# Optimization experiments

Hardware: AMD Instinct MI355X
Metric: run time of the kernel (lower is better)

Reference implementation:

```python
import jax, jax.numpy as jnp
import numpy as np

STATE_DIM, ACTION_DIM, HIDDEN, ACTOR_HIDDEN = 64, 8, 256, 256
B, T = 1024, 512


def _uniform(key, shape, bound):
    return jax.random.uniform(key, shape, jnp.float32, -bound, bound)


def setup_inputs() -> dict:
    key = jax.random.key(0)
    ks = jax.random.split(key, 12)
    k = 1.0 / np.sqrt(HIDDEN)  # PyTorch GRU/Linear init bound
    ka = 1.0 / np.sqrt(ACTOR_HIDDEN)
    return {
        "x_seq": jax.random.normal(ks[0], (B, T, STATE_DIM), jnp.float32),
        # GRU params (PyTorch layout: [3*H, in] with gate order r,z,n)
        "w_ih": _uniform(ks[1], (3 * HIDDEN, STATE_DIM), k),
        "w_hh": _uniform(ks[2], (3 * HIDDEN, HIDDEN), k),
        "b_ih": _uniform(ks[3], (3 * HIDDEN,), k),
        "b_hh": _uniform(ks[4], (3 * HIDDEN,), k),
        # base MLP
        "w_base": _uniform(ks[5], (ACTOR_HIDDEN, HIDDEN), k),
        "b_base": _uniform(ks[6], (ACTOR_HIDDEN,), k),
        # factorized heads
        "w_dir": _uniform(ks[7], (ACTION_DIM, ACTOR_HIDDEN), ka),
        "b_dir": _uniform(ks[8], (ACTION_DIM,), ka),
        "w_mag": _uniform(ks[9], (ACTION_DIM, ACTOR_HIDDEN), ka),
        "b_mag": _uniform(ks[10], (ACTION_DIM,), ka),
    }


def reference(x_seq, w_ih, w_hh, b_ih, b_hh, w_base, b_base, w_dir, b_dir, w_mag, b_mag):
    H = w_hh.shape[1]

    def step(h, x_t):
        gi = x_t @ w_ih.T + b_ih          # [B, 3H]
        gh = h @ w_hh.T + b_hh            # [B, 3H]
        i_r, i_z, i_n = jnp.split(gi, 3, axis=-1)
        h_r, h_z, h_n = jnp.split(gh, 3, axis=-1)
        r = jax.nn.sigmoid(i_r + h_r)
        z = jax.nn.sigmoid(i_z + h_z)
        n = jnp.tanh(i_n + r * h_n)
        h_new = (1.0 - z) * n + z * h
        return h_new, None

    h0 = jnp.zeros((x_seq.shape[0], H), x_seq.dtype)
    last, _ = jax.lax.scan(step, h0, jnp.swapaxes(x_seq, 0, 1))  # carry = h_T
    h = jax.nn.relu(last @ w_base.T + b_base)
    direction = jnp.tanh(h @ w_dir.T + b_dir)
    magnitude = jax.nn.sigmoid(h @ w_mag.T + b_mag)
    return direction * magnitude
```

## Files before the change

kernel.cpp:

```cpp
#include <hip/hip_runtime.h>

#define T_SEQ 512
#define HID 256

typedef _Float16 half8 __attribute__((ext_vector_type(8)));
typedef _Float16 half4 __attribute__((ext_vector_type(4)));
typedef float floatx4 __attribute__((ext_vector_type(4)));

#define OFF_GH 0
#define OFF_GI (OFF_GH + 384 * 512)
#define OFF_WB (OFF_GI + 96 * 512)
#define OFF_WD (OFF_WB + 128 * 512)
#define HSAVE_OFF_BYTES (4ull << 20)
#define GI_OFF_BYTES (6ull << 20)

#define MFMA16(A, B, C) __builtin_amdgcn_mfma_f32_16x16x32_f16(A, B, C, 0, 0, 0)

__device__ __forceinline__ float sigm(float x) { return 1.0f / (1.0f + __expf(-x)); }
__device__ __forceinline__ float tanh_fast(float x) {
  float e = __expf(2.0f * x);
  return 1.0f - 2.0f / (e + 1.0f);
}

__global__ void prep_kernel(const float* __restrict__ w_ih,
                            const float* __restrict__ w_hh,
                            const float* __restrict__ w_base,
                            const float* __restrict__ w_dir,
                            const float* __restrict__ w_mag,
                            _Float16* __restrict__ ws) {
  const int f = blockIdx.x;
  const int lane = threadIdx.x;
  const int col = lane & 15, quad = lane >> 4;
  const float* src;
  int n, k, ld;
  _Float16* dst;
  if (f < 384) {
    int nt = f % 6, kt = (f / 6) % 8, w = f / 48;
    n = (nt >> 1) * 256 + w * 32 + (nt & 1) * 16 + col;
    k = kt * 32 + quad * 8;
    src = w_hh; ld = 256;
    dst = ws + OFF_GH + ((w * 8 + kt) * 6 + nt) * 512 + lane * 8;
  } else if (f < 480) {
    int f2 = f - 384;
    int nt = f2 % 6, kt = (f2 / 6) % 2, w = f2 / 12;
    n = (nt >> 1) * 256 + w * 32 + (nt & 1) * 16 + col;
    k = kt * 32 + quad * 8;
    src = w_ih; ld = 64;
    dst = ws + OFF_GI + ((w * 2 + kt) * 6 + nt) * 512 + lane * 8;
  } else if (f < 608) {
    int f3 = f - 480;
    int nt = f3 % 2, kt = (f3 / 2) % 8, w = f3 / 16;
    n = w * 32 + nt * 16 + col;
    k = kt * 32 + quad * 8;
    src = w_base; ld = 256;
    dst = ws + OFF_WB + ((w * 8 + kt) * 2 + nt) * 512 + lane * 8;
  } else {
    int kt = f - 608;
    k = kt * 32 + quad * 8;
    ld = 256;
    if (col < 8) { src = w_dir; n = col; } else { src = w_mag; n = col - 8; }
    dst = ws + OFF_WD + kt * 512 + lane * 8;
  }
#pragma unroll
  for (int j = 0; j < 8; ++j)
    dst[j] = (_Float16)src[n * ld + k + j];
}

__global__ __launch_bounds__(512, 1)
void gi_prepass_kernel(const float* __restrict__ x_seq,
                       const float* __restrict__ b_ih,
                       const float* __restrict__ b_hh,
                       const _Float16* __restrict__ ws,
                       uint2* __restrict__ gi_out,
                       int t0, int nTq, int chunk) {
  const int tid = threadIdx.x;
  const int lane = tid & 63;
  const int w = tid >> 6;
  const int col = lane & 15;
  const int quad = lane >> 4;
  const int btile = blockIdx.x / nTq, tq = blockIdx.x % nTq;
  const int row0 = btile * 16;
  const int tstart = t0 + tq * 32;

  const half8* __restrict__ gip = (const half8*)(ws + OFF_GI) + w * (12 * 64);
  half8 wg[12];
#pragma unroll
  for (int f = 0; f < 12; ++f) wg[f] = gip[f * 64 + lane];

  float bias[6];
#pragma unroll
  for (int a = 0; a < 6; ++a) {
    const int c = w * 32 + (a & 1) * 16 + col;
    const int g = a >> 1;
    bias[a] = (g < 2) ? (b_ih[g * 256 + c] + b_hh[g * 256 + c]) : b_ih[512 + c];
  }

  const float* const xlane = x_seq + (size_t)(row0 + col) * (T_SEQ * 64) + quad * 8;
  uint2* const gout = gi_out + (size_t)btile * ((size_t)chunk * 3072) +
                      (size_t)w * 384 + lane;

  float4 xc[4], xn[4];
  {
    const float* p = xlane + (size_t)tstart * 64;
    xc[0] = *(const float4*)(p);
    xc[1] = *(const float4*)(p + 4);
    xc[2] = *(const float4*)(p + 32);
    xc[3] = *(const float4*)(p + 36);
  }

#pragma unroll 1
  for (int tt = 0; tt < 32; ++tt) {
    const int t = tstart + tt;
    if (tt + 1 < 32) {
      const float* p = xlane + (size_t)(t + 1) * 64;
      xn[0] = *(const float4*)(p);
      xn[1] = *(const float4*)(p + 4);
      xn[2] = *(const float4*)(p + 32);
      xn[3] = *(const float4*)(p + 36);
    }
    half8 ax0, ax1;
#pragma unroll
    for (int j = 0; j < 4; ++j) {
      ax0[j]     = (_Float16)((const float*)&xc[0])[j];
      ax0[4 + j] = (_Float16)((const float*)&xc[1])[j];
      ax1[j]     = (_Float16)((const float*)&xc[2])[j];
      ax1[4 + j] = (_Float16)((const float*)&xc[3])[j];
    }

    floatx4 acc[6];
#pragma unroll
    for (int a = 0; a < 6; ++a) acc[a] = (floatx4){0.f, 0.f, 0.f, 0.f};
#pragma unroll
    for (int nt = 0; nt < 6; ++nt) {
      acc[nt] = MFMA16(ax0, wg[nt], acc[nt]);
      acc[nt] = MFMA16(ax1, wg[6 + nt], acc[nt]);
    }

    uint2* gp = gout + (size_t)(t - t0) * 3072;
#pragma unroll
    for (int a = 0; a < 6; ++a) {
      union { uint2 u; half4 h; } pk;
#pragma unroll
      for (int r2 = 0; r2 < 4; ++r2)
        pk.h[r2] = (_Float16)(acc[a][r2] + bias[a]);
      gp[a * 64] = pk.u;
    }
#pragma unroll
    for (int i = 0; i < 4; ++i) xc[i] = xn[i];
  }
}

__global__ __launch_bounds__(512, 1)
void gru_main_kernel(const float* __restrict__ b_hh,
                     const float* __restrict__ b_base,
                     const float* __restrict__ b_dir,
                     const float* __restrict__ b_mag,
                     const _Float16* __restrict__ ws,
                     const uint2* __restrict__ gi_in,
                     float* __restrict__ hsave,
                     float* __restrict__ out,
                     int chunk, int first, int last) {
  __shared__ __align__(16) _Float16 hlin[2][4096];

  const int tid = threadIdx.x;
  const int lane = tid & 63;
  const int w = tid >> 6;
  const int col = lane & 15;
  const int quad = lane >> 4;
  const int row0 = blockIdx.x * 16;

  float bhn[2];
#pragma unroll
  for (int s = 0; s < 2; ++s) bhn[s] = b_hh[512 + w * 32 + s * 16 + col];

  float hreg[2][4];
  if (first) {
#pragma unroll
    for (int s = 0; s < 2; ++s)
#pragma unroll
      for (int r2 = 0; r2 < 4; ++r2) hreg[s][r2] = 0.0f;
    *(half8*)&hlin[0][tid * 8] = (half8)((_Float16)0.0f);
  } else {
    const float* hp = hsave + ((size_t)blockIdx.x * 512 + tid) * 8;
#pragma unroll
    for (int s = 0; s < 2; ++s) {
      const int inner = s * 16 + col;
      const int widx = w * 512 + (inner >> 3) * 128 + (col & 7);
#pragma unroll
      for (int r2 = 0; r2 < 4; ++r2) {
        hreg[s][r2] = hp[s * 4 + r2];
        hlin[0][widx + (quad * 4 + r2) * 8] = (_Float16)hreg[s][r2];
      }
    }
  }

  const half8* __restrict__ ghp = (const half8*)(ws + OFF_GH) + w * (48 * 64);
  const half8* __restrict__ wbp = (const half8*)(ws + OFF_WB) + w * (16 * 64);
  const half8* __restrict__ wdp = (const half8*)(ws + OFF_WD);

  half8 wreg[40];
#pragma unroll
  for (int f = 0; f < 40; ++f) wreg[f] = ghp[f * 64 + lane];

  const uint2* const gilane =
      gi_in + (size_t)blockIdx.x * ((size_t)chunk * 3072) + (size_t)w * 384 + lane;

#pragma unroll 1
  for (int tl = 0; tl < chunk; ++tl) {
    __syncthreads();
    const int cur = tl & 1;
    const _Float16* hc = hlin[cur];
    _Float16* hn = hlin[cur ^ 1];

    uint2 g[6];
    const uint2* gp = gilane + (size_t)tl * 3072;
#pragma unroll
    for (int a = 0; a < 6; ++a) g[a] = gp[a * 64];

    half8 st[8];
#pragma unroll
    for (int i = 0; i < 8; ++i) st[i] = ghp[(40 + i) * 64 + lane];

    half8 ah[8];
#pragma unroll
    for (int kt = 0; kt < 8; ++kt)
      ah[kt] = *(const half8*)&hc[kt * 512 + lane * 8];

    floatx4 acc[6];
#pragma unroll
    for (int a = 0; a < 6; ++a) acc[a] = (floatx4){0.f, 0.f, 0.f, 0.f};

#pragma unroll
    for (int f = 0; f < 40; ++f)
      acc[f % 6] = MFMA16(ah[f / 6], wreg[f], acc[f % 6]);
#pragma unroll
    for (int i = 0; i < 8; ++i) {
      const int f = 40 + i;
      acc[f % 6] = MFMA16(ah[f / 6], st[i], acc[f % 6]);
    }

#pragma unroll
    for (int s = 0; s < 2; ++s) {
      const int inner = s * 16 + col;
      const int widx = w * 512 + (inner >> 3) * 128 + (col & 7);
      union { uint2 u; half4 h; } gr, gz, gn;
      gr.u = g[0 + s]; gz.u = g[2 + s]; gn.u = g[4 + s];
#pragma unroll
      for (int r2 = 0; r2 < 4; ++r2) {
        const float rr = sigm(acc[0 + s][r2] + (float)gr.h[r2]);
        const float zz = sigm(acc[2 + s][r2] + (float)gz.h[r2]);
        const float nn = tanh_fast((float)gn.h[r2] + rr * (acc[4 + s][r2] + bhn[s]));
        const float hnew = zz * hreg[s][r2] + (1.0f - zz) * nn;
        hreg[s][r2] = hnew;
        hn[widx + (quad * 4 + r2) * 8] = (_Float16)hnew;
      }
    }
  }

  if (!last) {
    float* hp = hsave + ((size_t)blockIdx.x * 512 + tid) * 8;
#pragma unroll
    for (int s = 0; s < 2; ++s)
#pragma unroll
      for (int r2 = 0; r2 < 4; ++r2) hp[s * 4 + r2] = hreg[s][r2];
    return;
  }

  __syncthreads();
  {
    floatx4 ab[2];
    ab[0] = (floatx4){0.f, 0.f, 0.f, 0.f};
    ab[1] = (floatx4){0.f, 0.f, 0.f, 0.f};
#pragma unroll
    for (int kt = 0; kt < 8; ++kt) {
      const half8 ahh = *(const half8*)&hlin[0][kt * 512 + lane * 8];
      const half8* bp = wbp + kt * (2 * 64) + lane;
      ab[0] = MFMA16(ahh, bp[0],  ab[0]);
      ab[1] = MFMA16(ahh, bp[64], ab[1]);
    }
#pragma unroll
    for (int s = 0; s < 2; ++s) {
      const int inner = s * 16 + col;
      const int widx = w * 512 + (inner >> 3) * 128 + (col & 7);
      const float bb = b_base[w * 32 + inner];
#pragma unroll
      for (int r2 = 0; r2 < 4; ++r2) {
        const float v = ab[s][r2] + bb;
        hlin[1][widx + (quad * 4 + r2) * 8] = (_Float16)fmaxf(v, 0.0f);
      }
    }
  }
  __syncthreads();

  if (w == 0) {
    floatx4 ad = (floatx4){0.f, 0.f, 0.f, 0.f};
#pragma unroll
    for (int kt = 0; kt < 8; ++kt) {
      const half8 ahh = *(const half8*)&hlin[1][kt * 512 + lane * 8];
      ad = MFMA16(ahh, wdp[kt * 64 + lane], ad);
    }
    const float bd = (col < 8) ? b_dir[col] : b_mag[col - 8];
#pragma unroll
    for (int r2 = 0; r2 < 4; ++r2) {
      const float v = ad[r2] + bd;
      const float act = (col < 8) ? tanh_fast(v) : sigm(v);
      const float other = __shfl_xor(act, 8, 64);
      if (col < 8)
        out[(size_t)(row0 + quad * 4 + r2) * 8 + col] = act * other;
    }
  }
}

__global__ __launch_bounds__(512, 2)
void gru_head_fallback(const float* __restrict__ x_seq,
                       const float* __restrict__ b_ih,
                       const float* __restrict__ b_hh,
                       const float* __restrict__ b_base,
                       const float* __restrict__ b_dir,
                       const float* __restrict__ b_mag,
                       const _Float16* __restrict__ ws,
                       float* __restrict__ out) {
  __shared__ __align__(16) _Float16 hlin[2][4096];
  __shared__ __align__(16) _Float16 wlds[8][4096];

  const int tid = threadIdx.x;
  const int lane = tid & 63;
  const int w = tid >> 6;
  const int col = lane & 15;
  const int quad = lane >> 4;
  const int row0 = blockIdx.x * 16;

  *(half8*)&hlin[0][tid * 8] = (half8)((_Float16)0.0f);

  float br[2], bz[2], bin_[2], bhn[2];
#pragma unroll
  for (int s = 0; s < 2; ++s) {
    const int c = w * 32 + s * 16 + col;
    br[s] = b_ih[c] + b_hh[c];
    bz[s] = b_ih[256 + c] + b_hh[256 + c];
    bin_[s] = b_ih[512 + c];
    bhn[s] = b_hh[512 + c];
  }
  float hreg[2][4];
#pragma unroll
  for (int s = 0; s < 2; ++s)
#pragma unroll
    for (int r2 = 0; r2 < 4; ++r2) hreg[s][r2] = 0.0f;

  const half8* __restrict__ ghp = (const half8*)(ws + OFF_GH) + w * (48 * 64);
  const half8* __restrict__ gip = (const half8*)(ws + OFF_GI) + w * (12 * 64);
  const half8* __restrict__ wbp = (const half8*)(ws + OFF_WB) + w * (16 * 64);
  const half8* __restrict__ wdp = (const half8*)(ws + OFF_WD);

  half8 wreg[16];
#pragma unroll
  for (int f = 0; f < 16; ++f) wreg[f] = ghp[f * 64 + lane];
  _Float16* const wlw = wlds[w];
#pragma unroll
  for (int j = 0; j < 8; ++j)
    *(half8*)&wlw[j * 512 + lane * 8] = ghp[(16 + j) * 64 + lane];

  const float* const xlane = x_seq + ((size_t)(row0 + col) * T_SEQ) * 64 + quad * 8;
  float4 xc[4], xn[4];
  {
    const float* p = xlane;
    xc[0] = *(const float4*)(p);
    xc[1] = *(const float4*)(p + 4);
    xc[2] = *(const float4*)(p + 32);
    xc[3] = *(const float4*)(p + 36);
  }

  auto body = [&](int t, int tpre, int cur, float4* xcur, float4* xnext) {
    const int nxt = cur ^ 1;
    __syncthreads();
    half8 s1[6], s2[6];
#pragma unroll
    for (int i = 0; i < 6; ++i) s1[i] = ghp[(24 + i) * 64 + lane];
#pragma unroll
    for (int i = 0; i < 6; ++i) s2[i] = ghp[(30 + i) * 64 + lane];
    {
      const float* p = xlane + (size_t)tpre * 64;
      xnext[0] = *(const float4*)(p);
      xnext[1] = *(const float4*)(p + 4);
      xnext[2] = *(const float4*)(p + 32);
      xnext[3] = *(const float4*)(p + 36);
    }
    half8 ah[8];
#pragma unroll
    for (int kt = 0; kt < 8; ++kt)
      ah[kt] = *(const half8*)&hlin[cur][kt * 512 + lane * 8];
    half8 wl[8];
#pragma unroll
    for (int j = 0; j < 8; ++j)
      wl[j] = *(const half8*)&wlw[j * 512 + lane * 8];
    half8 ax0, ax1;
#pragma unroll
    for (int j = 0; j < 4; ++j) {
      ax0[j]     = (_Float16)((const float*)&xcur[0])[j];
      ax0[4 + j] = (_Float16)((const float*)&xcur[1])[j];
      ax1[j]     = (_Float16)((const float*)&xcur[2])[j];
      ax1[4 + j] = (_Float16)((const float*)&xcur[3])[j];
    }
    floatx4 acc[8];
#pragma unroll
    for (int i = 0; i < 8; ++i) acc[i] = (floatx4){0.f, 0.f, 0.f, 0.f};
#pragma unroll
    for (int f = 0; f < 16; ++f)
      acc[f % 6] = MFMA16(ah[f / 6], wreg[f], acc[f % 6]);
    half8 s3[6];
#pragma unroll
    for (int i = 0; i < 6; ++i) s3[i] = ghp[(36 + i) * 64 + lane];
#pragma unroll
    for (int j = 0; j < 8; ++j) {
      const int f = 16 + j;
      acc[f % 6] = MFMA16(ah[f / 6], wl[j], acc[f % 6]);
    }
#pragma unroll
    for (int i = 0; i < 6; ++i) {
      const int f = 24 + i;
      acc[f % 6] = MFMA16(ah[f / 6], s1[i], acc[f % 6]);
    }
    half8 s4[6];
#pragma unroll
    for (int i = 0; i < 6; ++i) s4[i] = ghp[(42 + i) * 64 + lane];
#pragma unroll
    for (int i = 0; i < 6; ++i) {
      const int f = 30 + i;
      acc[f % 6] = MFMA16(ah[f / 6], s2[i], acc[f % 6]);
    }
    half8 s5[6];
#pragma unroll
    for (int i = 0; i < 6; ++i) s5[i] = gip[i * 64 + lane];
#pragma unroll
    for (int i = 0; i < 6; ++i) {
      const int f = 36 + i;
      acc[f % 6] = MFMA16(ah[f / 6], s3[i], acc[f % 6]);
    }
    half8 s6[6];
#pragma unroll
    for (int i = 0; i < 6; ++i) s6[i] = gip[(6 + i) * 64 + lane];
#pragma unroll
    for (int i = 0; i < 6; ++i) {
      const int f = 42 + i;
      acc[f % 6] = MFMA16(ah[f / 6], s4[i], acc[f % 6]);
    }
#pragma unroll
    for (int i = 0; i < 6; ++i) {
      const int aidx = (i < 4) ? i : i + 2;
      acc[aidx] = MFMA16(ax0, s5[i], acc[aidx]);
    }
#pragma unroll
    for (int i = 0; i < 6; ++i) {
      const int aidx = (i < 4) ? i : i + 2;
      acc[aidx] = MFMA16(ax1, s6[i], acc[aidx]);
    }
#pragma unroll
    for (int s = 0; s < 2; ++s) {
      const int inner = s * 16 + col;
      const int widx = w * 512 + (inner >> 3) * 128 + (col & 7);
#pragma unroll
      for (int r2 = 0; r2 < 4; ++r2) {
        const float rr = sigm(acc[0 + s][r2] + br[s]);
        const float zz = sigm(acc[2 + s][r2] + bz[s]);
        const float nn = tanh_fast(acc[6 + s][r2] + bin_[s] + rr * (acc[4 + s][r2] + bhn[s]));
        const float hnew = zz * hreg[s][r2] + (1.0f - zz) * nn;
        hreg[s][r2] = hnew;
        hlin[nxt][widx + (quad * 4 + r2) * 8] = (_Float16)hnew;
      }
    }
  };

#pragma unroll 1
  for (int t = 0; t < T_SEQ; t += 2) {
    body(t, t + 1, 0, xc, xn);
    const int tp2 = (t + 2 < T_SEQ) ? (t + 2) : (T_SEQ - 1);
    body(t + 1, tp2, 1, xn, xc);
  }

  __syncthreads();
  {
    floatx4 ab[2];
    ab[0] = (floatx4){0.f, 0.f, 0.f, 0.f};
    ab[1] = (floatx4){0.f, 0.f, 0.f, 0.f};
#pragma unroll
    for (int kt = 0; kt < 8; ++kt) {
      const half8 ahh = *(const half8*)&hlin[0][kt * 512 + lane * 8];
      const half8* bp = wbp + kt * (2 * 64) + lane;
      ab[0] = MFMA16(ahh, bp[0],  ab[0]);
      ab[1] = MFMA16(ahh, bp[64], ab[1]);
    }
#pragma unroll
    for (int s = 0; s < 2; ++s) {
      const int inner = s * 16 + col;
      const int widx = w * 512 + (inner >> 3) * 128 + (col & 7);
      const float bb = b_base[w * 32 + inner];
#pragma unroll
      for (int r2 = 0; r2 < 4; ++r2) {
        const float v = ab[s][r2] + bb;
        hlin[1][widx + (quad * 4 + r2) * 8] = (_Float16)fmaxf(v, 0.0f);
      }
    }
  }
  __syncthreads();
  if (w == 0) {
    floatx4 ad = (floatx4){0.f, 0.f, 0.f, 0.f};
#pragma unroll
    for (int kt = 0; kt < 8; ++kt) {
      const half8 ahh = *(const half8*)&hlin[1][kt * 512 + lane * 8];
      ad = MFMA16(ahh, wdp[kt * 64 + lane], ad);
    }
    const float bd = (col < 8) ? b_dir[col] : b_mag[col - 8];
#pragma unroll
    for (int r2 = 0; r2 < 4; ++r2) {
      const float v = ad[r2] + bd;
      const float act = (col < 8) ? tanh_fast(v) : sigm(v);
      const float other = __shfl_xor(act, 8, 64);
      if (col < 8)
        out[(size_t)(row0 + quad * 4 + r2) * 8 + col] = act * other;
    }
  }
}

extern "C" void kernel_launch(void* const* d_in, const int* in_sizes, int n_in,
                              void* d_out, int out_size, void* d_ws, size_t ws_size,
                              hipStream_t stream) {
  const float* x_seq  = (const float*)d_in[0];
  const float* b_ih   = (const float*)d_in[3];
  const float* b_hh   = (const float*)d_in[4];
  const float* b_base = (const float*)d_in[6];
  const float* b_dir  = (const float*)d_in[8];
  const float* b_mag  = (const float*)d_in[10];
  _Float16* ws = (_Float16*)d_ws;
  float* out = (float*)d_out;

  hipLaunchKernelGGL(prep_kernel, dim3(616), dim3(64), 0, stream,
                     (const float*)d_in[1], (const float*)d_in[2],
                     (const float*)d_in[5], (const float*)d_in[7],
                     (const float*)d_in[9], ws);

  int chunk = 0;
  const int cand[3] = {128, 64, 32};
  for (int i = 0; i < 3; ++i) {
    const size_t need = GI_OFF_BYTES + 64ull * (size_t)cand[i] * 3072ull * 8ull;
    if (ws_size >= need) { chunk = cand[i]; break; }
  }

  if (chunk) {
    uint2* gi = (uint2*)((char*)d_ws + GI_OFF_BYTES);
    float* hsave = (float*)((char*)d_ws + HSAVE_OFF_BYTES);
    const int nchunks = T_SEQ / chunk;
    const int nTq = chunk / 32;
    for (int c = 0; c < nchunks; ++c) {
      hipLaunchKernelGGL(gi_prepass_kernel, dim3(64 * nTq), dim3(512), 0, stream,
                         x_seq, b_ih, b_hh, ws, gi, c * chunk, nTq, chunk);
      hipLaunchKernelGGL(gru_main_kernel, dim3(64), dim3(512), 0, stream,
                         b_hh, b_base, b_dir, b_mag, ws, gi, hsave, out,
                         chunk, (c == 0) ? 1 : 0, (c == nchunks - 1) ? 1 : 0);
    }
  } else {
    hipLaunchKernelGGL(gru_head_fallback, dim3(64), dim3(512), 0, stream,
                       x_seq, b_ih, b_hh, b_base, b_dir, b_mag, ws, out);
  }
}
```

Measured before the change: 1.912 ms.

## Fuse input projection into single persistent GRU kernel, drop chunked prepass

Replaces the chunked scheme, which alternated an input-projection prepass kernel with a recurrent kernel and staged gate inputs and hidden state through global memory, with one kernel of 64 blocks. That kernel computes x_t·W_ih with MFMA inside each timestep, keeps 40 of the 48 W_hh fragments plus all W_ih fragments in registers, streams the remaining 8 from global memory, and raises wave priority around the MFMA block. This removes the many kernel launches and the global round trips for gi and the saved hidden state. In exchange, every serial step now carries extra MFMAs and x loads on the critical path, and register pressure rises.

```diff
diff --git a/kernel.cpp b/kernel.cpp
--- a/kernel.cpp
+++ b/kernel.cpp
@@ -11,8 +11,6 @@
 #define OFF_GI (OFF_GH + 384 * 512)
 #define OFF_WB (OFF_GI + 96 * 512)
 #define OFF_WD (OFF_WB + 128 * 512)
-#define HSAVE_OFF_BYTES (4ull << 20)
-#define GI_OFF_BYTES (6ull << 20)
 
 #define MFMA16(A, B, C) __builtin_amdgcn_mfma_f32_16x16x32_f16(A, B, C, 0, 0, 0)
 
@@ -67,99 +65,14 @@
 }
 
 __global__ __launch_bounds__(512, 1)
-void gi_prepass_kernel(const float* __restrict__ x_seq,
-                       const float* __restrict__ b_ih,
-                       const float* __restrict__ b_hh,
-                       const _Float16* __restrict__ ws,
-                       uint2* __restrict__ gi_out,
-                       int t0, int nTq, int chunk) {
-  const int tid = threadIdx.x;
-  const int lane = tid & 63;
-  const int w = tid >> 6;
-  const int col = lane & 15;
-  const int quad = lane >> 4;
-  const int btile = blockIdx.x / nTq, tq = blockIdx.x % nTq;
-  const int row0 = btile * 16;
-  const int tstart = t0 + tq * 32;
-
-  const half8* __restrict__ gip = (const half8*)(ws + OFF_GI) + w * (12 * 64);
-  half8 wg[12];
-#pragma unroll
-  for (int f = 0; f < 12; ++f) wg[f] = gip[f * 64 + lane];
-
-  float bias[6];
-#pragma unroll
-  for (int a = 0; a < 6; ++a) {
-    const int c = w * 32 + (a & 1) * 16 + col;
-    const int g = a >> 1;
-    bias[a] = (g < 2) ? (b_ih[g * 256 + c] + b_hh[g * 256 + c]) : b_ih[512 + c];
-  }
-
-  const float* const xlane = x_seq + (size_t)(row0 + col) * (T_SEQ * 64) + quad * 8;
-  uint2* const gout = gi_out + (size_t)btile * ((size_t)chunk * 3072) +
-                      (size_t)w * 384 + lane;
-
-  float4 xc[4], xn[4];
-  {
-    const float* p = xlane + (size_t)tstart * 64;
-    xc[0] = *(const float4*)(p);
-    xc[1] = *(const float4*)(p + 4);
-    xc[2] = *(const float4*)(p + 32);
-    xc[3] = *(const float4*)(p + 36);
-  }
-
-#pragma unroll 1
-  for (int tt = 0; tt < 32; ++tt) {
-    const int t = tstart + tt;
-    if (tt + 1 < 32) {
-      const float* p = xlane + (size_t)(t + 1) * 64;
-      xn[0] = *(const float4*)(p);
-      xn[1] = *(const float4*)(p + 4);
-      xn[2] = *(const float4*)(p + 32);
-      xn[3] = *(const float4*)(p + 36);
-    }
-    half8 ax0, ax1;
-#pragma unroll
-    for (int j = 0; j < 4; ++j) {
-      ax0[j]     = (_Float16)((const float*)&xc[0])[j];
-      ax0[4 + j] = (_Float16)((const float*)&xc[1])[j];
-      ax1[j]     = (_Float16)((const float*)&xc[2])[j];
-      ax1[4 + j] = (_Float16)((const float*)&xc[3])[j];
-    }
-
-    floatx4 acc[6];
-#pragma unroll
-    for (int a = 0; a < 6; ++a) acc[a] = (floatx4){0.f, 0.f, 0.f, 0.f};
-#pragma unroll
-    for (int nt = 0; nt < 6; ++nt) {
-      acc[nt] = MFMA16(ax0, wg[nt], acc[nt]);
-      acc[nt] = MFMA16(ax1, wg[6 + nt], acc[nt]);
-    }
-
-    uint2* gp = gout + (size_t)(t - t0) * 3072;
-#pragma unroll
-    for (int a = 0; a < 6; ++a) {
-      union { uint2 u; half4 h; } pk;
-#pragma unroll
-      for (int r2 = 0; r2 < 4; ++r2)
-        pk.h[r2] = (_Float16)(acc[a][r2] + bias[a]);
-      gp[a * 64] = pk.u;
-    }
-#pragma unroll
-    for (int i = 0; i < 4; ++i) xc[i] = xn[i];
-  }
-}
-
-__global__ __launch_bounds__(512, 1)
-void gru_main_kernel(const float* __restrict__ b_hh,
-                     const float* __restrict__ b_base,
-                     const float* __restrict__ b_dir,
-                     const float* __restrict__ b_mag,
-                     const _Float16* __restrict__ ws,
-                     const uint2* __restrict__ gi_in,
-                     float* __restrict__ hsave,
-                     float* __restrict__ out,
-                     int chunk, int first, int last) {
+void gru_all_kernel(const float* __restrict__ x_seq,
+                    const float* __restrict__ b_ih,
+                    const float* __restrict__ b_hh,
+                    const float* __restrict__ b_base,
+                    const float* __restrict__ b_dir,
+                    const float* __restrict__ b_mag,
+                    const _Float16* __restrict__ ws,
+                    float* __restrict__ out) {
   __shared__ __align__(16) _Float16 hlin[2][4096];
 
   const int tid = threadIdx.x;
@@ -169,169 +82,6 @@
   const int quad = lane >> 4;
   const int row0 = blockIdx.x * 16;
 
-  float bhn[2];
-#pragma unroll
-  for (int s = 0; s < 2; ++s) bhn[s] = b_hh[512 + w * 32 + s * 16 + col];
-
-  float hreg[2][4];
-  if (first) {
-#pragma unroll
-    for (int s = 0; s < 2; ++s)
-#pragma unroll
-      for (int r2 = 0; r2 < 4; ++r2) hreg[s][r2] = 0.0f;
-    *(half8*)&hlin[0][tid * 8] = (half8)((_Float16)0.0f);
-  } else {
-    const float* hp = hsave + ((size_t)blockIdx.x * 512 + tid) * 8;
-#pragma unroll
-    for (int s = 0; s < 2; ++s) {
-      const int inner = s * 16 + col;
-      const int widx = w * 512 + (inner >> 3) * 128 + (col & 7);
-#pragma unroll
-      for (int r2 = 0; r2 < 4; ++r2) {
-        hreg[s][r2] = hp[s * 4 + r2];
-        hlin[0][widx + (quad * 4 + r2) * 8] = (_Float16)hreg[s][r2];
-      }
-    }
-  }
-
-  const half8* __restrict__ ghp = (const half8*)(ws + OFF_GH) + w * (48 * 64);
-  const half8* __restrict__ wbp = (const half8*)(ws + OFF_WB) + w * (16 * 64);
-  const half8* __restrict__ wdp = (const half8*)(ws + OFF_WD);
-
-  half8 wreg[40];
-#pragma unroll
-  for (int f = 0; f < 40; ++f) wreg[f] = ghp[f * 64 + lane];
-
-  const uint2* const gilane =
-      gi_in + (size_t)blockIdx.x * ((size_t)chunk * 3072) + (size_t)w * 384 + lane;
-
-#pragma unroll 1
-  for (int tl = 0; tl < chunk; ++tl) {
-    __syncthreads();
-    const int cur = tl & 1;
-    const _Float16* hc = hlin[cur];
-    _Float16* hn = hlin[cur ^ 1];
-
-    uint2 g[6];
-    const uint2* gp = gilane + (size_t)tl * 3072;
-#pragma unroll
-    for (int a = 0; a < 6; ++a) g[a] = gp[a * 64];
-
-    half8 st[8];
-#pragma unroll
-    for (int i = 0; i < 8; ++i) st[i] = ghp[(40 + i) * 64 + lane];
-
-    half8 ah[8];
-#pragma unroll
-    for (int kt = 0; kt < 8; ++kt)
-      ah[kt] = *(const half8*)&hc[kt * 512 + lane * 8];
-
-    floatx4 acc[6];
-#pragma unroll
-    for (int a = 0; a < 6; ++a) acc[a] = (floatx4){0.f, 0.f, 0.f, 0.f};
-
-#pragma unroll
-    for (int f = 0; f < 40; ++f)
-      acc[f % 6] = MFMA16(ah[f / 6], wreg[f], acc[f % 6]);
-#pragma unroll
-    for (int i = 0; i < 8; ++i) {
-      const int f = 40 + i;
-      acc[f % 6] = MFMA16(ah[f / 6], st[i], acc[f % 6]);
-    }
-
-#pragma unroll
-    for (int s = 0; s < 2; ++s) {
-      const int inner = s * 16 + col;
-      const int widx = w * 512 + (inner >> 3) * 128 + (col & 7);
-      union { uint2 u; half4 h; } gr, gz, gn;
-      gr.u = g[0 + s]; gz.u = g[2 + s]; gn.u = g[4 + s];
-#pragma unroll
-      for (int r2 = 0; r2 < 4; ++r2) {
-        const float rr = sigm(acc[0 + s][r2] + (float)gr.h[r2]);
-        const float zz = sigm(acc[2 + s][r2] + (float)gz.h[r2]);
-        const float nn = tanh_fast((float)gn.h[r2] + rr * (acc[4 + s][r2] + bhn[s]));
-        const float hnew = zz * hreg[s][r2] + (1.0f - zz) * nn;
-        hreg[s][r2] = hnew;
-        hn[widx + (quad * 4 + r2) * 8] = (_Float16)hnew;
-      }
-    }
-  }
-
-  if (!last) {
-    float* hp = hsave + ((size_t)blockIdx.x * 512 + tid) * 8;
-#pragma unroll
-    for (int s = 0; s < 2; ++s)
-#pragma unroll
-      for (int r2 = 0; r2 < 4; ++r2) hp[s * 4 + r2] = hreg[s][r2];
-    return;
-  }
-
-  __syncthreads();
-  {
-    floatx4 ab[2];
-    ab[0] = (floatx4){0.f, 0.f, 0.f, 0.f};
-    ab[1] = (floatx4){0.f, 0.f, 0.f, 0.f};
-#pragma unroll
-    for (int kt = 0; kt < 8; ++kt) {
-      const half8 ahh = *(const half8*)&hlin[0][kt * 512 + lane * 8];
-      const half8* bp = wbp + kt * (2 * 64) + lane;
-      ab[0] = MFMA16(ahh, bp[0],  ab[0]);
-      ab[1] = MFMA16(ahh, bp[64], ab[1]);
-    }
-#pragma unroll
-    for (int s = 0; s < 2; ++s) {
-      const int inner = s * 16 + col;
-      const int widx = w * 512 + (inner >> 3) * 128 + (col & 7);
-      const float bb = b_base[w * 32 + inner];
-#pragma unroll
-      for (int r2 = 0; r2 < 4; ++r2) {
-        const float v = ab[s][r2] + bb;
-        hlin[1][widx + (quad * 4 + r2) * 8] = (_Float16)fmaxf(v, 0.0f);
-      }
-    }
-  }
-  __syncthreads();
-
-  if (w == 0) {
-    floatx4 ad = (floatx4){0.f, 0.f, 0.f, 0.f};
-#pragma unroll
-    for (int kt = 0; kt < 8; ++kt) {
-      const half8 ahh = *(const half8*)&hlin[1][kt * 512 + lane * 8];
-      ad = MFMA16(ahh, wdp[kt * 64 + lane], ad);
-    }
-    const float bd = (col < 8) ? b_dir[col] : b_mag[col - 8];
-#pragma unroll
-    for (int r2 = 0; r2 < 4; ++r2) {
-      const float v = ad[r2] + bd;
-      const float act = (col < 8) ? tanh_fast(v) : sigm(v);
-      const float other = __shfl_xor(act, 8, 64);
-      if (col < 8)
-        out[(size_t)(row0 + quad * 4 + r2) * 8 + col] = act * other;
-    }
-  }
-}
-
-__global__ __launch_bounds__(512, 2)
-void gru_head_fallback(const float* __restrict__ x_seq,
-                       const float* __restrict__ b_ih,
-                       const float* __restrict__ b_hh,
-                       const float* __restrict__ b_base,
-                       const float* __restrict__ b_dir,
-                       const float* __restrict__ b_mag,
-                       const _Float16* __restrict__ ws,
-                       float* __restrict__ out) {
-  __shared__ __align__(16) _Float16 hlin[2][4096];
-  __shared__ __align__(16) _Float16 wlds[8][4096];
-
-  const int tid = threadIdx.x;
-  const int lane = tid & 63;
-  const int w = tid >> 6;
-  const int col = lane & 15;
-  const int quad = lane >> 4;
-  const int row0 = blockIdx.x * 16;
-
-  *(half8*)&hlin[0][tid * 8] = (half8)((_Float16)0.0f);
-
   float br[2], bz[2], bin_[2], bhn[2];
 #pragma unroll
   for (int s = 0; s < 2; ++s) {
@@ -341,26 +91,28 @@
     bin_[s] = b_ih[512 + c];
     bhn[s] = b_hh[512 + c];
   }
+
   float hreg[2][4];
 #pragma unroll
   for (int s = 0; s < 2; ++s)
 #pragma unroll
     for (int r2 = 0; r2 < 4; ++r2) hreg[s][r2] = 0.0f;
+  *(half8*)&hlin[0][tid * 8] = (half8)((_Float16)0.0f);
 
   const half8* __restrict__ ghp = (const half8*)(ws + OFF_GH) + w * (48 * 64);
   const half8* __restrict__ gip = (const half8*)(ws + OFF_GI) + w * (12 * 64);
   const half8* __restrict__ wbp = (const half8*)(ws + OFF_WB) + w * (16 * 64);
   const half8* __restrict__ wdp = (const half8*)(ws + OFF_WD);
 
-  half8 wreg[16];
-#pragma unroll
-  for (int f = 0; f < 16; ++f) wreg[f] = ghp[f * 64 + lane];
-  _Float16* const wlw = wlds[w];
-#pragma unroll
-  for (int j = 0; j < 8; ++j)
-    *(half8*)&wlw[j * 512 + lane * 8] = ghp[(16 + j) * 64 + lane];
-
-  const float* const xlane = x_seq + ((size_t)(row0 + col) * T_SEQ) * 64 + quad * 8;
+  half8 wreg[40];
+#pragma unroll
+  for (int f = 0; f < 40; ++f) wreg[f] = ghp[f * 64 + lane];
+  half8 wg[12];
+#pragma unroll
+  for (int f = 0; f < 12; ++f) wg[f] = gip[f * 64 + lane];
+
+  const float* const xlane =
+      x_seq + (size_t)(row0 + col) * (T_SEQ * 64) + quad * 8;
   float4 xc[4], xn[4];
   {
     const float* p = xlane;
@@ -370,14 +122,14 @@
     xc[3] = *(const float4*)(p + 36);
   }
 
-  auto body = [&](int t, int tpre, int cur, float4* xcur, float4* xnext) {
-    const int nxt = cur ^ 1;
+  auto body = [&](int tpre, int cur, float4* xcur, float4* xnext) {
     __syncthreads();
-    half8 s1[6], s2[6];
-#pragma unroll
-    for (int i = 0; i < 6; ++i) s1[i] = ghp[(24 + i) * 64 + lane];
-#pragma unroll
-    for (int i = 0; i < 6; ++i) s2[i] = ghp[(30 + i) * 64 + lane];
+    const _Float16* hc = hlin[cur];
+    _Float16* hn = hlin[cur ^ 1];
+
+    half8 st[8];
+#pragma unroll
+    for (int i = 0; i < 8; ++i) st[i] = ghp[(40 + i) * 64 + lane];
     {
       const float* p = xlane + (size_t)tpre * 64;
       xnext[0] = *(const float4*)(p);
@@ -385,14 +137,12 @@
       xnext[2] = *(const float4*)(p + 32);
       xnext[3] = *(const float4*)(p + 36);
     }
+
     half8 ah[8];
 #pragma unroll
     for (int kt = 0; kt < 8; ++kt)
-      ah[kt] = *(const half8*)&hlin[cur][kt * 512 + lane * 8];
-    half8 wl[8];
-#pragma unroll
-    for (int j = 0; j < 8; ++j)
-      wl[j] = *(const half8*)&wlw[j * 512 + lane * 8];
+      ah[kt] = *(const half8*)&hc[kt * 512 + lane * 8];
+
     half8 ax0, ax1;
 #pragma unroll
     for (int j = 0; j < 4; ++j) {
@@ -401,59 +151,31 @@
       ax1[j]     = (_Float16)((const float*)&xcur[2])[j];
       ax1[4 + j] = (_Float16)((const float*)&xcur[3])[j];
     }
+
     floatx4 acc[8];
 #pragma unroll
     for (int i = 0; i < 8; ++i) acc[i] = (floatx4){0.f, 0.f, 0.f, 0.f};
-#pragma unroll
-    for (int f = 0; f < 16; ++f)
+
+    __builtin_amdgcn_s_setprio(1);
+#pragma unroll
+    for (int f = 0; f < 40; ++f)
       acc[f % 6] = MFMA16(ah[f / 6], wreg[f], acc[f % 6]);
-    half8 s3[6];
-#pragma unroll
-    for (int i = 0; i < 6; ++i) s3[i] = ghp[(36 + i) * 64 + lane];
-#pragma unroll
-    for (int j = 0; j < 8; ++j) {
-      const int f = 16 + j;
-      acc[f % 6] = MFMA16(ah[f / 6], wl[j], acc[f % 6]);
-    }
-#pragma unroll
-    for (int i = 0; i < 6; ++i) {
-      const int f = 24 + i;
-      acc[f % 6] = MFMA16(ah[f / 6], s1[i], acc[f % 6]);
-    }
-    half8 s4[6];
-#pragma unroll
-    for (int i = 0; i < 6; ++i) s4[i] = ghp[(42 + i) * 64 + lane];
-#pragma unroll
-    for (int i = 0; i < 6; ++i) {
-      const int f = 30 + i;
-      acc[f % 6] = MFMA16(ah[f / 6], s2[i], acc[f % 6]);
-    }
-    half8 s5[6];
-#pragma unroll
-    for (int i = 0; i < 6; ++i) s5[i] = gip[i * 64 + lane];
-#pragma unroll
-    for (int i = 0; i < 6; ++i) {
-      const int f = 36 + i;
-      acc[f % 6] = MFMA16(ah[f / 6], s3[i], acc[f % 6]);
-    }
-    half8 s6[6];
-#pragma unroll
-    for (int i = 0; i < 6; ++i) s6[i] = gip[(6 + i) * 64 + lane];
-#pragma unroll
-    for (int i = 0; i < 6; ++i) {
-      const int f = 42 + i;
-      acc[f % 6] = MFMA16(ah[f / 6], s4[i], acc[f % 6]);
-    }
-#pragma unroll
-    for (int i = 0; i < 6; ++i) {
-      const int aidx = (i < 4) ? i : i + 2;
-      acc[aidx] = MFMA16(ax0, s5[i], acc[aidx]);
-    }
-#pragma unroll
-    for (int i = 0; i < 6; ++i) {
-      const int aidx = (i < 4) ? i : i + 2;
-      acc[aidx] = MFMA16(ax1, s6[i], acc[aidx]);
-    }
+#pragma unroll
+    for (int kt2 = 0; kt2 < 2; ++kt2) {
+      const half8 ax = kt2 ? ax1 : ax0;
+#pragma unroll
+      for (int nt = 0; nt < 6; ++nt) {
+        const int aidx = (nt < 4) ? nt : nt + 2;
+        acc[aidx] = MFMA16(ax, wg[kt2 * 6 + nt], acc[aidx]);
+      }
+    }
+#pragma unroll
+    for (int i = 0; i < 8; ++i) {
+      const int f = 40 + i;
+      acc[f % 6] = MFMA16(ah[f / 6], st[i], acc[f % 6]);
+    }
+    __builtin_amdgcn_s_setprio(0);
+
 #pragma unroll
     for (int s = 0; s < 2; ++s) {
       const int inner = s * 16 + col;
@@ -462,19 +184,20 @@
       for (int r2 = 0; r2 < 4; ++r2) {
         const float rr = sigm(acc[0 + s][r2] + br[s]);
         const float zz = sigm(acc[2 + s][r2] + bz[s]);
-        const float nn = tanh_fast(acc[6 + s][r2] + bin_[s] + rr * (acc[4 + s][r2] + bhn[s]));
+        const float nn =
+            tanh_fast(acc[6 + s][r2] + bin_[s] + rr * (acc[4 + s][r2] + bhn[s]));
         const float hnew = zz * hreg[s][r2] + (1.0f - zz) * nn;
         hreg[s][r2] = hnew;
-        hlin[nxt][widx + (quad * 4 + r2) * 8] = (_Float16)hnew;
+        hn[widx + (quad * 4 + r2) * 8] = (_Float16)hnew;
       }
     }
   };
 
 #pragma unroll 1
   for (int t = 0; t < T_SEQ; t += 2) {
-    body(t, t + 1, 0, xc, xn);
+    body(t + 1, 0, xc, xn);
     const int tp2 = (t + 2 < T_SEQ) ? (t + 2) : (T_SEQ - 1);
-    body(t + 1, tp2, 1, xn, xc);
+    body(tp2, 1, xn, xc);
   }
 
   __syncthreads();
@@ -502,6 +225,7 @@
     }
   }
   __syncthreads();
+
   if (w == 0) {
     floatx4 ad = (floatx4){0.f, 0.f, 0.f, 0.f};
 #pragma unroll
@@ -538,27 +262,6 @@
                      (const float*)d_in[5], (const float*)d_in[7],
                      (const float*)d_in[9], ws);
 
-  int chunk = 0;
-  const int cand[3] = {128, 64, 32};
-  for (int i = 0; i < 3; ++i) {
-    const size_t need = GI_OFF_BYTES + 64ull * (size_t)cand[i] * 3072ull * 8ull;
-    if (ws_size >= need) { chunk = cand[i]; break; }
-  }
-
-  if (chunk) {
-    uint2* gi = (uint2*)((char*)d_ws + GI_OFF_BYTES);
-    float* hsave = (float*)((char*)d_ws + HSAVE_OFF_BYTES);
-    const int nchunks = T_SEQ / chunk;
-    const int nTq = chunk / 32;
-    for (int c = 0; c < nchunks; ++c) {
-      hipLaunchKernelGGL(gi_prepass_kernel, dim3(64 * nTq), dim3(512), 0, stream,
-                         x_seq, b_ih, b_hh, ws, gi, c * chunk, nTq, chunk);
-      hipLaunchKernelGGL(gru_main_kernel, dim3(64), dim3(512), 0, stream,
-                         b_hh, b_base, b_dir, b_mag, ws, gi, hsave, out,
-                         chunk, (c == 0) ? 1 : 0, (c == nchunks - 1) ? 1 : 0);
-    }
-  } else {
-    hipLaunchKernelGGL(gru_head_fallback, dim3(64), dim3(512), 0, stream,
-                       x_seq, b_ih, b_hh, b_base, b_dir, b_mag, ws, out);
-  }
-}
+  hipLaunchKernelGGL(gru_all_kernel, dim3(64), dim3(512), 0, stream,
+                     x_seq, b_ih, b_hh, b_base, b_dir, b_mag, ws, out);
+}
```

Result: slower. 4.308 ms (+125.3%).
